# Kernel tuning notes

Measured on AMD Instinct MI355X. Metric: run time of the kernel, lower is better.

## Reference

```python
import jax, jax.numpy as jnp
import numpy as np

EPS = 1e-5

def layer_norm(x, g, b):
    mu = jnp.mean(x, axis=-1, keepdims=True)
    var = jnp.mean((x - mu) ** 2, axis=-1, keepdims=True)
    return (x - mu) * jax.lax.rsqrt(var + EPS) * g + b

def setup_inputs() -> dict:
    key = jax.random.key(0)
    ks = jax.random.split(key, 12)
    P, D_IN, H, D_OUT, N = 2097152, 3, 64, 128, 65536
    x = jax.random.normal(ks[0], (P, D_IN), dtype=jnp.float32)
    batch_idx = jax.random.randint(ks[1], (P,), 0, N, dtype=jnp.int64)
    # mlp1: Linear(3,64) -> LN(64) -> ReLU -> Linear(64,64)
    W1 = jax.random.normal(ks[2], (D_IN, H), dtype=jnp.float32) * (1.0 / np.sqrt(D_IN))
    b1 = jnp.zeros((H,), jnp.float32)
    g1 = jnp.ones((H,), jnp.float32)
    be1 = jnp.zeros((H,), jnp.float32)
    W2 = jax.random.normal(ks[3], (H, H), dtype=jnp.float32) * (1.0 / np.sqrt(H))
    b2 = jnp.zeros((H,), jnp.float32)
    # mlp2: Linear(64,128) -> LN(128) -> ReLU -> Linear(128,128)
    W3 = jax.random.normal(ks[4], (H, D_OUT), dtype=jnp.float32) * (1.0 / np.sqrt(H))
    b3 = jnp.zeros((D_OUT,), jnp.float32)
    g2 = jnp.ones((D_OUT,), jnp.float32)
    be2 = jnp.zeros((D_OUT,), jnp.float32)
    W4 = jax.random.normal(ks[5], (D_OUT, D_OUT), dtype=jnp.float32) * (1.0 / np.sqrt(D_OUT))
    b4 = jnp.zeros((D_OUT,), jnp.float32)
    return {"x": x, "batch_idx": batch_idx, "num_nodes": N,
            "W1": W1, "b1": b1, "g1": g1, "be1": be1, "W2": W2, "b2": b2,
            "W3": W3, "b3": b3, "g2": g2, "be2": be2, "W4": W4, "b4": b4}

def reference(x, batch_idx, num_nodes, W1, b1, g1, be1, W2, b2, W3, b3, g2, be2, W4, b4):
    # per-point MLP1: [P,3] -> [P,64]
    h = jax.nn.relu(layer_norm(x @ W1 + b1, g1, be1)) @ W2 + b2
    # scatter_max pooling over unsorted batch_idx -> [num_nodes, 64]
    seg = jax.ops.segment_max(h, batch_idx, num_segments=num_nodes)
    counts = jax.ops.segment_sum(jnp.ones((h.shape[0],), h.dtype), batch_idx, num_segments=num_nodes)
    # torch_scatter.scatter_max leaves empty segments at 0
    seg = jnp.where(counts[:, None] > 0, seg, 0.0)
    # MLP2: [N,64] -> [N,128]
    out = jax.nn.relu(layer_norm(seg @ W3 + b3, g2, be2)) @ W4 + b4
    return out
```

## Files before the change

kernel.cpp:

```cpp
#include <hip/hip_runtime.h>
#include <hip/hip_bf16.h>
#include <math.h>

#define EPS_LN 1e-5f

typedef __attribute__((ext_vector_type(8))) short bf16x8;
typedef __attribute__((ext_vector_type(4))) float f32x4;
typedef __attribute__((ext_vector_type(2))) unsigned short u16x2;
typedef __attribute__((ext_vector_type(4))) unsigned int u32x4;

__device__ __forceinline__ unsigned short f2bf(float f) {
    __hip_bfloat16 h = __float2bfloat16(f);
    return *reinterpret_cast<unsigned short*>(&h);
}
__device__ __forceinline__ float bf2f(unsigned short u) {
    return __uint_as_float(((unsigned)u) << 16);
}
__device__ __forceinline__ unsigned short ok16(float f) {
    unsigned short t = f2bf(f);
    unsigned short mask = (unsigned short)(((short)t) >> 15);
    return (unsigned short)(t ^ (unsigned short)(mask | 0x8000u));
}
__device__ __forceinline__ float decseg(unsigned o) {
    if (o == 0u) return 0.f;
    unsigned k = o >> 16;
    unsigned h = (k & 0x8000u) ? (k & 0x7FFFu) : (~k & 0xFFFFu);
    return bf2f((unsigned short)h);
}

__global__ __launch_bounds__(256) void prep_kernel(
    const float* __restrict__ W1, const float* __restrict__ b1,
    const float* __restrict__ g1, const float* __restrict__ be1,
    const float* __restrict__ W2,
    const float* __restrict__ W3, const float* __restrict__ W4,
    float* __restrict__ pW1e, float* __restrict__ pGB, float* __restrict__ pSG,
    unsigned short* __restrict__ pW2t,
    unsigned short* __restrict__ W3th, unsigned short* __restrict__ W3tl,
    unsigned short* __restrict__ W4th, unsigned short* __restrict__ W4tl)
{
    const int tid = threadIdx.x;
    if (tid < 64) {
        pW1e[4 * tid + 0] = W1[tid];
        pW1e[4 * tid + 1] = W1[64 + tid];
        pW1e[4 * tid + 2] = W1[128 + tid];
        pW1e[4 * tid + 3] = b1[tid];
        pGB[2 * tid + 0] = g1[tid];
        pGB[2 * tid + 1] = be1[tid];
    }
    if (tid >= 64 && tid < 78) {
        const int t = tid - 64;
        auto wcomp = [&](int k, int i) -> float {
            return (i < 3) ? W1[i * 64 + k] : b1[k];
        };
        if (t < 4) {
            float s = 0.f;
            for (int k = 0; k < 64; k++) s += wcomp(k, t);
            pSG[t] = s;
        } else {
            const int pi[10] = {0,0,0,0,1,1,1,2,2,3};
            const int pj[10] = {0,1,2,3,1,2,3,2,3,3};
            int p = t - 4;
            float s = 0.f;
            for (int k = 0; k < 64; k++) s += wcomp(k, pi[p]) * wcomp(k, pj[p]);
            pSG[4 + p] = s;
        }
    }
    for (int i = tid; i < 4096; i += 256) {
        int k = i >> 6, n = i & 63;
        pW2t[n * 72 + k] = f2bf(W2[i]);
    }
    for (int i = tid; i < 64 * 8; i += 256) {
        int n = i >> 3, k = 64 + (i & 7);
        pW2t[n * 72 + k] = 0;
    }
    for (int i = tid; i < 8192; i += 256) {
        int k = i >> 7, n = i & 127;
        float w = W3[k * 128 + n];
        unsigned short h = f2bf(w);
        W3th[n * 64 + k] = h;
        W3tl[n * 64 + k] = f2bf(w - bf2f(h));
    }
    for (int i = tid; i < 16384; i += 256) {
        int k = i >> 7, n = i & 127;
        float w = W4[k * 128 + n];
        unsigned short h = f2bf(w);
        W4th[n * 128 + k] = h;
        W4tl[n * 128 + k] = f2bf(w - bf2f(h));
    }
}

__global__ __launch_bounds__(256) void s1_count(const int* __restrict__ bidx,
                                                unsigned* __restrict__ blockHist, int P) {
    __shared__ unsigned hist[2048];
    const int tid = threadIdx.x;
    for (int i = tid; i < 2048; i += 256) hist[i] = 0;
    __syncthreads();
    const int base = blockIdx.x * 4096;
#pragma unroll
    for (int j = 0; j < 4; j++) {
        const int p0 = base + j * 1024 + tid * 4;
        if (p0 + 3 < P) {
            int4 n4 = *(const int4*)(bidx + p0);
            atomicAdd(&hist[((unsigned)n4.x) >> 5], 1u);
            atomicAdd(&hist[((unsigned)n4.y) >> 5], 1u);
            atomicAdd(&hist[((unsigned)n4.z) >> 5], 1u);
            atomicAdd(&hist[((unsigned)n4.w) >> 5], 1u);
        } else {
            for (int p = p0; p < P && p < p0 + 4; p++)
                atomicAdd(&hist[((unsigned)bidx[p]) >> 5], 1u);
        }
    }
    __syncthreads();
    unsigned* dst = blockHist + (size_t)blockIdx.x * 2048;
    for (int i = tid; i < 2048; i += 256) dst[i] = hist[i];
}

__global__ __launch_bounds__(256) void s2a_total(const unsigned* __restrict__ blockHist,
                                                 unsigned* __restrict__ binTotal, int nblk) {
    const int bin = blockIdx.x;
    const int tid = threadIdx.x;
    unsigned s = 0;
    for (int b = tid; b < nblk; b += 256) s += blockHist[(size_t)b * 2048 + bin];
    for (int off = 32; off; off >>= 1) s += __shfl_down(s, off);
    __shared__ unsigned ws[4];
    if ((tid & 63) == 0) ws[tid >> 6] = s;
    __syncthreads();
    if (tid == 0) binTotal[bin] = ws[0] + ws[1] + ws[2] + ws[3];
}

__global__ __launch_bounds__(1024) void s2b_scan(const unsigned* __restrict__ binTotal,
                                                 unsigned* __restrict__ partBase,
                                                 int nparts, int P) {
    __shared__ unsigned wtot[16];
    const int t = threadIdx.x;
    const unsigned c0 = (2 * t < nparts) ? binTotal[2 * t] : 0u;
    const unsigned c1 = (2 * t + 1 < nparts) ? binTotal[2 * t + 1] : 0u;
    const unsigned s = c0 + c1;
    unsigned v = s;
    const int lane = t & 63;
    for (int off = 1; off < 64; off <<= 1) {
        unsigned u = __shfl_up(v, off);
        if (lane >= off) v += u;
    }
    if (lane == 63) wtot[t >> 6] = v;
    __syncthreads();
    if (t == 0) {
        unsigned a = 0;
        for (int w = 0; w < 16; w++) { unsigned tmp = wtot[w]; wtot[w] = a; a += tmp; }
    }
    __syncthreads();
    const unsigned excl = wtot[t >> 6] + (v - s);
    if (2 * t < nparts) partBase[2 * t] = excl;
    if (2 * t + 1 < nparts) partBase[2 * t + 1] = excl + c0;
    if (t == 0) partBase[nparts] = (unsigned)P;
}

__global__ __launch_bounds__(256) void s2c_cursor(unsigned* __restrict__ blockHist,
                                                  const unsigned* __restrict__ partBase,
                                                  int nblk) {
    __shared__ unsigned wt0[4], wb0[4], wt1[4], wb1[4], tot0s;
    const int bin = blockIdx.x;
    const int tid = threadIdx.x;
    const int lane = tid & 63;
    const unsigned c0 = (tid < nblk) ? blockHist[(size_t)tid * 2048 + bin] : 0u;
    const unsigned c1 = (tid + 256 < nblk) ? blockHist[(size_t)(tid + 256) * 2048 + bin] : 0u;

    unsigned v0 = c0;
    for (int off = 1; off < 64; off <<= 1) {
        unsigned u = __shfl_up(v0, off);
        if (lane >= off) v0 += u;
    }
    if (lane == 63) wt0[tid >> 6] = v0;
    unsigned v1 = c1;
    for (int off = 1; off < 64; off <<= 1) {
        unsigned u = __shfl_up(v1, off);
        if (lane >= off) v1 += u;
    }
    if (lane == 63) wt1[tid >> 6] = v1;
    __syncthreads();
    if (tid == 0) {
        unsigned a = 0;
        for (int i = 0; i < 4; i++) { unsigned tmp = wt0[i]; wb0[i] = a; a += tmp; }
        tot0s = a;
        a = 0;
        for (int i = 0; i < 4; i++) { unsigned tmp = wt1[i]; wb1[i] = a; a += tmp; }
    }
    __syncthreads();
    const unsigned pb = partBase[bin];
    const unsigned e0 = pb + wb0[tid >> 6] + (v0 - c0);
    const unsigned e1 = pb + tot0s + wb1[tid >> 6] + (v1 - c1);
    if (tid < nblk) blockHist[(size_t)tid * 2048 + bin] = e0;
    if (tid + 256 < nblk) blockHist[(size_t)(tid + 256) * 2048 + bin] = e1;
}

__global__ __launch_bounds__(256) void s3_scatter(const int* __restrict__ bidx,
                                                  const float* __restrict__ x,
                                                  const unsigned* __restrict__ blockCursor,
                                                  float4* __restrict__ xb, int P) {
    __shared__ unsigned cur[2048];
    const int tid = threadIdx.x;
    const unsigned* src = blockCursor + (size_t)blockIdx.x * 2048;
    for (int i = tid; i < 2048; i += 256) cur[i] = src[i];
    __syncthreads();
    const int base = blockIdx.x * 4096;
#pragma unroll
    for (int j = 0; j < 4; j++) {
        const int p0 = base + j * 1024 + tid * 4;
        if (p0 + 3 < P) {
            int4 n4 = *(const int4*)(bidx + p0);
            const float4* xv = (const float4*)(x + 3 * (size_t)p0);
            float4 a = xv[0], b = xv[1], c = xv[2];
            const float xs[12] = {a.x, a.y, a.z, a.w, b.x, b.y, b.z, b.w,
                                  c.x, c.y, c.z, c.w};
            const unsigned nn[4] = {(unsigned)n4.x, (unsigned)n4.y,
                                    (unsigned)n4.z, (unsigned)n4.w};
#pragma unroll
            for (int u = 0; u < 4; u++) {
                const unsigned dst = atomicAdd(&cur[nn[u] >> 5], 1u);
                xb[dst] = make_float4(xs[3 * u], xs[3 * u + 1], xs[3 * u + 2],
                                      __uint_as_float(nn[u]));
            }
        } else {
            for (int u = 0; u < 4; u++) {
                const int p = p0 + u;
                if (p < P) {
                    const unsigned n = (unsigned)bidx[p];
                    const unsigned dst = atomicAdd(&cur[n >> 5], 1u);
                    xb[dst] = make_float4(x[3 * p], x[3 * p + 1], x[3 * p + 2],
                                          __uint_as_float(n));
                }
            }
        }
    }
}

__global__ __launch_bounds__(256) void s4_csr(const unsigned* __restrict__ partBase,
                                              unsigned* __restrict__ offsets,
                                              float4* __restrict__ xb, int N) {
    __shared__ float4 stage[1600];
    __shared__ unsigned hist[32], cur[32];
    const int tid = threadIdx.x;
    const int p = blockIdx.x;
    const unsigned start = partBase[p], end = partBase[p + 1];
    unsigned cnt = end - start;
    if (cnt > 1600u) cnt = 1600u;
    if (tid < 32) hist[tid] = 0;
    __syncthreads();
    for (unsigned k = tid; k < cnt; k += 256) {
        float4 r = xb[start + k];
        stage[k] = r;
        atomicAdd(&hist[__float_as_uint(r.w) & 31u], 1u);
    }
    __syncthreads();
    if (tid < 64) {
        const unsigned c = (tid < 32) ? hist[tid] : 0u;
        unsigned v = c;
        for (int off = 1; off < 32; off <<= 1) {
            unsigned u = __shfl_up(v, off);
            if (tid >= off) v += u;
        }
        if (tid < 32) {
            const unsigned excl = v - c;
            const int node = p * 32 + tid;
            if (node < N) offsets[node] = start + excl;
            cur[tid] = start + excl;
            if (node == N - 1) offsets[N] = start + excl + c;
        }
    }
    __syncthreads();
    for (unsigned k = tid; k < cnt; k += 256) {
        float4 r = stage[k];
        const unsigned dst = atomicAdd(&cur[__float_as_uint(r.w) & 31u], 1u);
        xb[dst] = r;
    }
}

__global__ __launch_bounds__(256, 4) void fused_mlp1_pool_kernel(
    const float4* __restrict__ xb, const unsigned* __restrict__ offsets,
    const float* __restrict__ pW1e, const float* __restrict__ pGB,
    const float* __restrict__ pSG, const unsigned short* __restrict__ pW2t,
    const float* __restrict__ b2,
    unsigned* __restrict__ segord, int P)
{
    __shared__ __align__(16) unsigned short shbt[64 * 260];
    __shared__ unsigned sn01[2];

    const int tid  = threadIdx.x;
    const int wv   = tid >> 6;
    const int lane = tid & 63;
    const int m    = lane & 15;
    const int quad = lane >> 4;
    const int base = blockIdx.x * 256;
    const int pos  = base + tid;
    const bool valid = (pos < P);

    bf16x8 bfrag[4][2];
    float bc[4];
#pragma unroll
    for (int nt = 0; nt < 4; nt++) {
        bc[nt] = b2[nt * 16 + m];
#pragma unroll
        for (int s = 0; s < 2; s++)
            bfrag[nt][s] = *reinterpret_cast<const bf16x8*>(
                &pW2t[(nt * 16 + m) * 72 + s * 32 + quad * 8]);
    }

    float x0 = 0.f, x1 = 0.f, x2 = 0.f;
    if (valid) {
        float4 v = xb[pos];
        x0 = v.x; x1 = v.y; x2 = v.z;
        unsigned node = __float_as_uint(v.w);
        if (tid == 0) sn01[0] = node;
        if (tid == 255 || pos == P - 1) sn01[1] = node;
    }

    float rs, r2;
    {
        const float S0 = pSG[0], S1 = pSG[1], S2 = pSG[2], S3 = pSG[3];
        const float g00 = pSG[4], g01 = pSG[5], g02 = pSG[6], g03 = pSG[7];
        const float g11 = pSG[8], g12 = pSG[9], g13 = pSG[10];
        const float g22 = pSG[11], g23 = pSG[12], g33 = pSG[13];

        const float mu = fmaf(S0, x0, fmaf(S1, x1, fmaf(S2, x2, S3))) * (1.f / 64.f);
        float q = g33;
        q = fmaf(g00, x0 * x0, q);
        q = fmaf(g11, x1 * x1, q);
        q = fmaf(g22, x2 * x2, q);
        float c = fmaf(g01, x1, fmaf(g02, x2, g03));
        q = fmaf(2.f * x0, c, q);
        q = fmaf(2.f * x1, fmaf(g12, x2, g13), q);
        q = fmaf(2.f * x2, g23, q);
        float var = q * (1.f / 64.f) - mu * mu;
        var = var > 0.f ? var : 0.f;
        rs = rsqrtf(var + EPS_LN);
        r2 = -mu * rs;
    }

    float xr0[4], xr1[4], xr2[4], rsr[4], r2r[4];
#pragma unroll
    for (int rt = 0; rt < 4; rt++) {
        const int src = rt * 16 + m;
        xr0[rt] = __shfl(x0, src);
        xr1[rt] = __shfl(x1, src);
        xr2[rt] = __shfl(x2, src);
        rsr[rt] = __shfl(rs, src);
        r2r[rt] = __shfl(r2, src);
    }

    u32x4 afr[4][2];
    {
        const float4* pw = (const float4*)pW1e;
        const float2* pg = (const float2*)pGB;
#pragma unroll
        for (int s = 0; s < 2; s++) {
#pragma unroll
            for (int up = 0; up < 4; up++) {
                const int ch = s * 32 + quad * 8 + up * 2;
                const float4 wA = pw[ch], wB = pw[ch + 1];
                const float2 gA = pg[ch], gB = pg[ch + 1];
#pragma unroll
                for (int rt = 0; rt < 4; rt++) {
                    float y0 = fmaf(xr0[rt], wA.x, fmaf(xr1[rt], wA.y,
                               fmaf(xr2[rt], wA.z, wA.w)));
                    float y1 = fmaf(xr0[rt], wB.x, fmaf(xr1[rt], wB.y,
                               fmaf(xr2[rt], wB.z, wB.w)));
                    float a0 = fmaf(fmaf(y0, rsr[rt], r2r[rt]), gA.x, gA.y);
                    float a1 = fmaf(fmaf(y1, rsr[rt], r2r[rt]), gB.x, gB.y);
                    a0 = a0 > 0.f ? a0 : 0.f;
                    a1 = a1 > 0.f ? a1 : 0.f;
                    afr[rt][s][up] = (unsigned)f2bf(a0) | ((unsigned)f2bf(a1) << 16);
                }
            }
        }
    }

#pragma unroll
    for (int rt = 0; rt < 4; rt++) {
        const int orow = wv * 64 + rt * 16 + quad * 4;
        const bf16x8 af0 = __builtin_bit_cast(bf16x8, afr[rt][0]);
        const bf16x8 af1 = __builtin_bit_cast(bf16x8, afr[rt][1]);
#pragma unroll
        for (int nt = 0; nt < 4; nt++) {
            f32x4 acc = {bc[nt], bc[nt], bc[nt], bc[nt]};
            acc = __builtin_amdgcn_mfma_f32_16x16x32_bf16(af0, bfrag[nt][0], acc, 0, 0, 0);
            acc = __builtin_amdgcn_mfma_f32_16x16x32_bf16(af1, bfrag[nt][1], acc, 0, 0, 0);
            const int col = nt * 16 + m;
            uint2 pk;
            pk.x = (unsigned)ok16(acc[0]) | ((unsigned)ok16(acc[1]) << 16);
            pk.y = (unsigned)ok16(acc[2]) | ((unsigned)ok16(acc[3]) << 16);
            *reinterpret_cast<uint2*>(&shbt[col * 260 + orow]) = pk;
        }
    }
    __syncthreads();

    const int nValid = (P - base < 256) ? (P - base) : 256;
    if (nValid <= 0) return;
    const unsigned n0 = sn01[0];
    const unsigned n1 = sn01[1];
    const unsigned bEnd = (unsigned)(base + nValid);
    const int wave = tid >> 6;
    const int ch   = tid & 63;
    const unsigned short* rowp = &shbt[ch * 260];

    for (unsigned n = n0 + (unsigned)wave; n <= n1; n += 4) {
        const unsigned s = offsets[n];
        const unsigned e = offsets[n + 1];
        int lo = (int)(s > (unsigned)base ? s : (unsigned)base) - base;
        int hi = (int)(e < bEnd ? e : bEnd) - base;
        if (hi <= lo) continue;
        u16x2 accv = {0, 0};
        unsigned short accs = 0;
        for (int r = lo & ~3; r < hi; r += 4) {
            uint2 d = *reinterpret_cast<const uint2*>(rowp + r);
            if (r >= lo && r + 4 <= hi) {
                u16x2 a = __builtin_bit_cast(u16x2, d.x);
                u16x2 b = __builtin_bit_cast(u16x2, d.y);
                accv = __builtin_elementwise_max(accv, __builtin_elementwise_max(a, b));
            } else {
                unsigned short v0 = (unsigned short)(d.x & 0xFFFFu);
                unsigned short v1 = (unsigned short)(d.x >> 16);
                unsigned short v2 = (unsigned short)(d.y & 0xFFFFu);
                unsigned short v3 = (unsigned short)(d.y >> 16);
                if (r     >= lo && r     < hi && v0 > accs) accs = v0;
                if (r + 1 >= lo && r + 1 < hi && v1 > accs) accs = v1;
                if (r + 2 >= lo && r + 2 < hi && v2 > accs) accs = v2;
                if (r + 3 >= lo && r + 3 < hi && v3 > accs) accs = v3;
            }
        }
        unsigned short k = accv.x > accv.y ? accv.x : accv.y;
        if (accs > k) k = accs;
        const unsigned key = ((unsigned)k) << 16;
        unsigned* dst = &segord[(size_t)n * 64 + ch];
        if (s >= (unsigned)base && e <= bEnd) *dst = key;
        else atomicMax(dst, key);
    }
}

__global__ __launch_bounds__(256) void mlp2_mfma_kernel(
    const unsigned* __restrict__ segord,
    const unsigned short* __restrict__ W3th, const unsigned short* __restrict__ W3tl,
    const unsigned short* __restrict__ W4th, const unsigned short* __restrict__ W4tl,
    const float* __restrict__ b3, const float* __restrict__ g2,
    const float* __restrict__ be2, const float* __restrict__ b4,
    float* __restrict__ out, int N)
{
    __shared__ __align__(16) unsigned short sa2[32 * 72];
    __shared__ __align__(16) float st[32 * 132];
    __shared__ __align__(16) unsigned short suh[32 * 136];
    __shared__ __align__(16) unsigned short sul[32 * 136];
    __shared__ float2 sred[32][8];
    __shared__ float sg2[128], sbe2[128];

    const int tid  = threadIdx.x;
    const int wv   = tid >> 6;
    const int lane = tid & 63;
    const int m    = lane & 15;
    const int quad = lane >> 4;

    if (tid < 128) { sg2[tid] = g2[tid]; sbe2[tid] = be2[tid]; }

    bf16x8 fw3h[2][2], fw3l[2][2];
    bf16x8 fw4h[2][4], fw4l[2][4];
    float bias3[2], bias4[2];
#pragma unroll
    for (int nti = 0; nti < 2; nti++) {
        const int nrow = (wv * 2 + nti) * 16 + m;
        bias3[nti] = b3[nrow];
        bias4[nti] = b4[nrow];
#pragma unroll
        for (int ks = 0; ks < 2; ks++) {
            fw3h[nti][ks] = *reinterpret_cast<const bf16x8*>(&W3th[nrow * 64 + ks * 32 + quad * 8]);
            fw3l[nti][ks] = *reinterpret_cast<const bf16x8*>(&W3tl[nrow * 64 + ks * 32 + quad * 8]);
        }
#pragma unroll
        for (int ks = 0; ks < 4; ks++) {
            fw4h[nti][ks] = *reinterpret_cast<const bf16x8*>(&W4th[nrow * 128 + ks * 32 + quad * 8]);
            fw4l[nti][ks] = *reinterpret_cast<const bf16x8*>(&W4tl[nrow * 128 + ks * 32 + quad * 8]);
        }
    }
    __syncthreads();

    for (int nb = blockIdx.x * 32; nb < N; nb += gridDim.x * 32) {
        {
            const int node = tid >> 3;
            const int k8   = (tid & 7) * 8;
            const uint4* sp = (const uint4*)&segord[(size_t)(nb + node) * 64 + k8];
            uint4 q0 = sp[0], q1 = sp[1];
            bf16x8 v;
            v[0] = (short)f2bf(decseg(q0.x));
            v[1] = (short)f2bf(decseg(q0.y));
            v[2] = (short)f2bf(decseg(q0.z));
            v[3] = (short)f2bf(decseg(q0.w));
            v[4] = (short)f2bf(decseg(q1.x));
            v[5] = (short)f2bf(decseg(q1.y));
            v[6] = (short)f2bf(decseg(q1.z));
            v[7] = (short)f2bf(decseg(q1.w));
            *reinterpret_cast<bf16x8*>(&sa2[node * 72 + k8]) = v;
        }
        __syncthreads();

#pragma unroll
        for (int mt = 0; mt < 2; mt++) {
            bf16x8 a0 = *reinterpret_cast<const bf16x8*>(&sa2[(mt * 16 + m) * 72 + quad * 8]);
            bf16x8 a1 = *reinterpret_cast<const bf16x8*>(&sa2[(mt * 16 + m) * 72 + 32 + quad * 8]);
#pragma unroll
            for (int nti = 0; nti < 2; nti++) {
                f32x4 acc = {bias3[nti], bias3[nti], bias3[nti], bias3[nti]};
                acc = __builtin_amdgcn_mfma_f32_16x16x32_bf16(a0, fw3h[nti][0], acc, 0, 0, 0);
                acc = __builtin_amdgcn_mfma_f32_16x16x32_bf16(a1, fw3h[nti][1], acc, 0, 0, 0);
                acc = __builtin_amdgcn_mfma_f32_16x16x32_bf16(a0, fw3l[nti][0], acc, 0, 0, 0);
                acc = __builtin_amdgcn_mfma_f32_16x16x32_bf16(a1, fw3l[nti][1], acc, 0, 0, 0);
#pragma unroll
                for (int r = 0; r < 4; r++)
                    st[(mt * 16 + quad * 4 + r) * 132 + (wv * 2 + nti) * 16 + m] = acc[r];
            }
        }
        __syncthreads();

        {
            const int node = tid >> 3;
            const int seg  = tid & 7;
            const float4* rp = (const float4*)&st[node * 132 + seg * 16];
            float4 v0 = rp[0], v1 = rp[1], v2 = rp[2], v3 = rp[3];
            float s1 = v0.x + v0.y + v0.z + v0.w + v1.x + v1.y + v1.z + v1.w
                     + v2.x + v2.y + v2.z + v2.w + v3.x + v3.y + v3.z + v3.w;
            float s2 = 0.f;
            s2 = fmaf(v0.x, v0.x, s2); s2 = fmaf(v0.y, v0.y, s2); s2 = fmaf(v0.z, v0.z, s2); s2 = fmaf(v0.w, v0.w, s2);
            s2 = fmaf(v1.x, v1.x, s2); s2 = fmaf(v1.y, v1.y, s2); s2 = fmaf(v1.z, v1.z, s2); s2 = fmaf(v1.w, v1.w, s2);
            s2 = fmaf(v2.x, v2.x, s2); s2 = fmaf(v2.y, v2.y, s2); s2 = fmaf(v2.z, v2.z, s2); s2 = fmaf(v2.w, v2.w, s2);
            s2 = fmaf(v3.x, v3.x, s2); s2 = fmaf(v3.y, v3.y, s2); s2 = fmaf(v3.z, v3.z, s2); s2 = fmaf(v3.w, v3.w, s2);
            sred[node][seg] = make_float2(s1, s2);
            __syncthreads();

            float t1 = 0.f, t2 = 0.f;
#pragma unroll
            for (int i = 0; i < 8; i++) { float2 r = sred[node][i]; t1 += r.x; t2 += r.y; }
            const float mu  = t1 * (1.f / 128.f);
            float var = t2 * (1.f / 128.f) - mu * mu;
            var = var > 0.f ? var : 0.f;
            const float rsd = rsqrtf(var + EPS_LN);

            float tv[16] = {v0.x, v0.y, v0.z, v0.w, v1.x, v1.y, v1.z, v1.w,
                            v2.x, v2.y, v2.z, v2.w, v3.x, v3.y, v3.z, v3.w};
            bf16x8 vh[2], vl[2];
#pragma unroll
            for (int i = 0; i < 16; i++) {
                const int j = seg * 16 + i;
                float u = fmaf((tv[i] - mu) * rsd, sg2[j], sbe2[j]);
                u = u > 0.f ? u : 0.f;
                unsigned short uh = f2bf(u);
                unsigned short ul = f2bf(u - bf2f(uh));
                vh[i >> 3][i & 7] = (short)uh;
                vl[i >> 3][i & 7] = (short)ul;
            }
            *reinterpret_cast<bf16x8*>(&suh[node * 136 + seg * 16])     = vh[0];
            *reinterpret_cast<bf16x8*>(&suh[node * 136 + seg * 16 + 8]) = vh[1];
            *reinterpret_cast<bf16x8*>(&sul[node * 136 + seg * 16])     = vl[0];
            *reinterpret_cast<bf16x8*>(&sul[node * 136 + seg * 16 + 8]) = vl[1];
        }
        __syncthreads();

#pragma unroll
        for (int mt = 0; mt < 2; mt++) {
            bf16x8 ah[4], al[4];
#pragma unroll
            for (int ks = 0; ks < 4; ks++) {
                ah[ks] = *reinterpret_cast<const bf16x8*>(&suh[(mt * 16 + m) * 136 + ks * 32 + quad * 8]);
                al[ks] = *reinterpret_cast<const bf16x8*>(&sul[(mt * 16 + m) * 136 + ks * 32 + quad * 8]);
            }
#pragma unroll
            for (int nti = 0; nti < 2; nti++) {
                f32x4 acc = {bias4[nti], bias4[nti], bias4[nti], bias4[nti]};
#pragma unroll
                for (int ks = 0; ks < 4; ks++) {
                    acc = __builtin_amdgcn_mfma_f32_16x16x32_bf16(ah[ks], fw4h[nti][ks], acc, 0, 0, 0);
                    acc = __builtin_amdgcn_mfma_f32_16x16x32_bf16(al[ks], fw4h[nti][ks], acc, 0, 0, 0);
                    acc = __builtin_amdgcn_mfma_f32_16x16x32_bf16(ah[ks], fw4l[nti][ks], acc, 0, 0, 0);
                }
#pragma unroll
                for (int r = 0; r < 4; r++) {
                    const int node = nb + mt * 16 + quad * 4 + r;
                    if (node < N)
                        out[(size_t)node * 128 + (wv * 2 + nti) * 16 + m] = acc[r];
                }
            }
        }
        __syncthreads();
    }
}

extern "C" void kernel_launch(void* const* d_in, const int* in_sizes, int n_in,
                              void* d_out, int out_size, void* d_ws, size_t ws_size,
                              hipStream_t stream) {
    const float* x    = (const float*)d_in[0];
    const int*   bidx = (const int*)d_in[1];
    const float* W1  = (const float*)d_in[3];
    const float* b1  = (const float*)d_in[4];
    const float* g1  = (const float*)d_in[5];
    const float* be1 = (const float*)d_in[6];
    const float* W2  = (const float*)d_in[7];
    const float* b2  = (const float*)d_in[8];
    const float* W3  = (const float*)d_in[9];
    const float* b3  = (const float*)d_in[10];
    const float* g2  = (const float*)d_in[11];
    const float* be2 = (const float*)d_in[12];
    const float* W4  = (const float*)d_in[13];
    const float* b4  = (const float*)d_in[14];

    const int P = in_sizes[0] / 3;
    const int N = out_size / 128;
    const int nparts = (N + 31) >> 5;
    const int nblk   = (P + 4095) / 4096;

    uintptr_t w = (uintptr_t)d_ws;
    auto align = [](uintptr_t v) { return (v + 255) & ~(uintptr_t)255; };
    unsigned* blockHist = (unsigned*)align(w);     w = (uintptr_t)(blockHist + (size_t)nblk * 2048);
    unsigned* binTotal  = (unsigned*)align(w);     w = (uintptr_t)(binTotal  + 2048);
    unsigned* partBase  = (unsigned*)align(w);     w = (uintptr_t)(partBase  + 2049);
    unsigned* offsets   = (unsigned*)align(w);     w = (uintptr_t)(offsets   + N + 1);
    float4*   xb        = (float4*)align(w);       w = (uintptr_t)(xb        + P);
    unsigned* segord    = (unsigned*)align(w);     w = (uintptr_t)(segord    + (size_t)N * 64);
    float*    pW1e      = (float*)align(w);        w = (uintptr_t)(pW1e      + 256);
    float*    pGB       = (float*)align(w);        w = (uintptr_t)(pGB       + 128);
    float*    pSG       = (float*)align(w);        w = (uintptr_t)(pSG       + 16);
    unsigned short* pW2t = (unsigned short*)align(w); w = (uintptr_t)(pW2t + 64 * 72);
    unsigned short* W3th = (unsigned short*)align(w); w = (uintptr_t)(W3th + 128 * 64);
    unsigned short* W3tl = (unsigned short*)align(w); w = (uintptr_t)(W3tl + 128 * 64);
    unsigned short* W4th = (unsigned short*)align(w); w = (uintptr_t)(W4th + 128 * 128);
    unsigned short* W4tl = (unsigned short*)align(w); w = (uintptr_t)(W4tl + 128 * 128);

    hipMemsetAsync(segord, 0, (size_t)N * 64 * sizeof(unsigned), stream);

    prep_kernel<<<1, 256, 0, stream>>>(W1, b1, g1, be1, W2, W3, W4,
                                       pW1e, pGB, pSG, pW2t, W3th, W3tl, W4th, W4tl);

    s1_count<<<nblk, 256, 0, stream>>>(bidx, blockHist, P);
    s2a_total<<<nparts, 256, 0, stream>>>(blockHist, binTotal, nblk);
    s2b_scan<<<1, 1024, 0, stream>>>(binTotal, partBase, nparts, P);
    s2c_cursor<<<nparts, 256, 0, stream>>>(blockHist, partBase, nblk);
    s3_scatter<<<nblk, 256, 0, stream>>>(bidx, x, blockHist, xb, P);
    s4_csr<<<nparts, 256, 0, stream>>>(partBase, offsets, xb, N);

    fused_mlp1_pool_kernel<<<(P + 255) / 256, 256, 0, stream>>>(
        xb, offsets, pW1e, pGB, pSG, pW2t, b2, segord, P);

    mlp2_mfma_kernel<<<512, 256, 0, stream>>>(
        segord, W3th, W3tl, W4th, W4tl, b3, g2, be2, b4, (float*)d_out, N);
}
```

Before: 340.3 us.

## Compute MLP1 first layer in packed fp16 and use fp16 MFMA

Moves the Linear(3,64)+LayerNorm+ReLU elementwise work in the fused MLP1/pool kernel from scalar fp32 FMAs to packed fp16x2 FMAs. The weights, gamma and beta are pre-packed as half pairs, and x, rs and r2 are shuffled as duplicated half pairs. The second linear layer switches from bf16 MFMA to f16 MFMA. The order-preserving key encoding is now done on packed 32-bit words, and the occupancy hint is lowered from 4 to 3. The aim is to halve the VALU instruction count of the per-point activation pass, at the cost of fp16 range and precision risk in the LayerNorm and ReLU intermediates.

```diff
diff --git a/kernel.cpp b/kernel.cpp
--- a/kernel.cpp
+++ b/kernel.cpp
@@ -8,6 +8,8 @@
 typedef __attribute__((ext_vector_type(4))) float f32x4;
 typedef __attribute__((ext_vector_type(2))) unsigned short u16x2;
 typedef __attribute__((ext_vector_type(4))) unsigned int u32x4;
+typedef _Float16 f16x2 __attribute__((ext_vector_type(2)));
+typedef _Float16 f16x8 __attribute__((ext_vector_type(8)));
 
 __device__ __forceinline__ unsigned short f2bf(float f) {
     __hip_bfloat16 h = __float2bfloat16(f);
@@ -16,10 +18,12 @@
 __device__ __forceinline__ float bf2f(unsigned short u) {
     return __uint_as_float(((unsigned)u) << 16);
 }
-__device__ __forceinline__ unsigned short ok16(float f) {
-    unsigned short t = f2bf(f);
-    unsigned short mask = (unsigned short)(((short)t) >> 15);
-    return (unsigned short)(t ^ (unsigned short)(mask | 0x8000u));
+__device__ __forceinline__ unsigned short f2h(float f) {
+    _Float16 h = (_Float16)f;
+    return __builtin_bit_cast(unsigned short, h);
+}
+__device__ __forceinline__ unsigned okpk(unsigned v) {
+    return v ^ (0x80008000u | (((v >> 15) & 0x00010001u) * 0x7FFFu));
 }
 __device__ __forceinline__ float decseg(unsigned o) {
     if (o == 0u) return 0.f;
@@ -27,25 +31,36 @@
     unsigned h = (k & 0x8000u) ? (k & 0x7FFFu) : (~k & 0xFFFFu);
     return bf2f((unsigned short)h);
 }
+__device__ __forceinline__ f16x2 bc16(unsigned u) {
+    return __builtin_bit_cast(f16x2, u);
+}
 
 __global__ __launch_bounds__(256) void prep_kernel(
     const float* __restrict__ W1, const float* __restrict__ b1,
     const float* __restrict__ g1, const float* __restrict__ be1,
     const float* __restrict__ W2,
     const float* __restrict__ W3, const float* __restrict__ W4,
-    float* __restrict__ pW1e, float* __restrict__ pGB, float* __restrict__ pSG,
+    unsigned short* __restrict__ pW1f, float* __restrict__ pSG,
     unsigned short* __restrict__ pW2t,
     unsigned short* __restrict__ W3th, unsigned short* __restrict__ W3tl,
     unsigned short* __restrict__ W4th, unsigned short* __restrict__ W4tl)
 {
     const int tid = threadIdx.x;
-    if (tid < 64) {
-        pW1e[4 * tid + 0] = W1[tid];
-        pW1e[4 * tid + 1] = W1[64 + tid];
-        pW1e[4 * tid + 2] = W1[128 + tid];
-        pW1e[4 * tid + 3] = b1[tid];
-        pGB[2 * tid + 0] = g1[tid];
-        pGB[2 * tid + 1] = be1[tid];
+    if (tid < 32) {
+        const int c0 = 2 * tid, c1 = 2 * tid + 1;
+        auto pk2 = [&](float a, float b) -> unsigned {
+            return (unsigned)f2h(a) | ((unsigned)f2h(b) << 16);
+        };
+        uint4 qa;
+        qa.x = pk2(W1[c0],        W1[c1]);
+        qa.y = pk2(W1[64 + c0],   W1[64 + c1]);
+        qa.z = pk2(W1[128 + c0],  W1[128 + c1]);
+        qa.w = pk2(b1[c0],        b1[c1]);
+        uint2 qb;
+        qb.x = pk2(g1[c0],  g1[c1]);
+        qb.y = pk2(be1[c0], be1[c1]);
+        *reinterpret_cast<uint4*>(&pW1f[tid * 16])     = qa;
+        *reinterpret_cast<uint2*>(&pW1f[tid * 16 + 8]) = qb;
     }
     if (tid >= 64 && tid < 78) {
         const int t = tid - 64;
@@ -67,7 +82,7 @@
     }
     for (int i = tid; i < 4096; i += 256) {
         int k = i >> 6, n = i & 63;
-        pW2t[n * 72 + k] = f2bf(W2[i]);
+        pW2t[n * 72 + k] = f2h(W2[i]);
     }
     for (int i = tid; i < 64 * 8; i += 256) {
         int n = i >> 3, k = 64 + (i & 7);
@@ -275,11 +290,10 @@
     }
 }
 
-__global__ __launch_bounds__(256, 4) void fused_mlp1_pool_kernel(
+__global__ __launch_bounds__(256, 3) void fused_mlp1_pool_kernel(
     const float4* __restrict__ xb, const unsigned* __restrict__ offsets,
-    const float* __restrict__ pW1e, const float* __restrict__ pGB,
-    const float* __restrict__ pSG, const unsigned short* __restrict__ pW2t,
-    const float* __restrict__ b2,
+    const unsigned short* __restrict__ pW1f, const float* __restrict__ pSG,
+    const unsigned short* __restrict__ pW2t, const float* __restrict__ b2,
     unsigned* __restrict__ segord, int P)
 {
     __shared__ __align__(16) unsigned short shbt[64 * 260];
@@ -293,17 +307,6 @@
     const int base = blockIdx.x * 256;
     const int pos  = base + tid;
     const bool valid = (pos < P);
-
-    bf16x8 bfrag[4][2];
-    float bc[4];
-#pragma unroll
-    for (int nt = 0; nt < 4; nt++) {
-        bc[nt] = b2[nt * 16 + m];
-#pragma unroll
-        for (int s = 0; s < 2; s++)
-            bfrag[nt][s] = *reinterpret_cast<const bf16x8*>(
-                &pW2t[(nt * 16 + m) * 72 + s * 32 + quad * 8]);
-    }
 
     float x0 = 0.f, x1 = 0.f, x2 = 0.f;
     if (valid) {
@@ -336,58 +339,66 @@
         r2 = -mu * rs;
     }
 
-    float xr0[4], xr1[4], xr2[4], rsr[4], r2r[4];
+    const unsigned px0 = (unsigned)f2h(x0) * 0x00010001u;
+    const unsigned px1 = (unsigned)f2h(x1) * 0x00010001u;
+    const unsigned px2 = (unsigned)f2h(x2) * 0x00010001u;
+    const unsigned prs = (unsigned)f2h(rs) * 0x00010001u;
+    const unsigned pr2 = (unsigned)f2h(r2) * 0x00010001u;
+
+    f16x8 bfrag[4][2];
+    float bc[4];
+#pragma unroll
+    for (int nt = 0; nt < 4; nt++) {
+        bc[nt] = b2[nt * 16 + m];
+#pragma unroll
+        for (int s = 0; s < 2; s++)
+            bfrag[nt][s] = *reinterpret_cast<const f16x8*>(
+                &pW2t[(nt * 16 + m) * 72 + s * 32 + quad * 8]);
+    }
+
+    const f16x2 fz = (f16x2)((_Float16)0.f);
+
 #pragma unroll
     for (int rt = 0; rt < 4; rt++) {
         const int src = rt * 16 + m;
-        xr0[rt] = __shfl(x0, src);
-        xr1[rt] = __shfl(x1, src);
-        xr2[rt] = __shfl(x2, src);
-        rsr[rt] = __shfl(rs, src);
-        r2r[rt] = __shfl(r2, src);
-    }
-
-    u32x4 afr[4][2];
-    {
-        const float4* pw = (const float4*)pW1e;
-        const float2* pg = (const float2*)pGB;
+        const f16x2 vx0 = bc16((unsigned)__shfl((int)px0, src));
+        const f16x2 vx1 = bc16((unsigned)__shfl((int)px1, src));
+        const f16x2 vx2 = bc16((unsigned)__shfl((int)px2, src));
+        const f16x2 vrs = bc16((unsigned)__shfl((int)prs, src));
+        const f16x2 vr2 = bc16((unsigned)__shfl((int)pr2, src));
+
+        unsigned aw[2][4];
 #pragma unroll
         for (int s = 0; s < 2; s++) {
 #pragma unroll
             for (int up = 0; up < 4; up++) {
-                const int ch = s * 32 + quad * 8 + up * 2;
-                const float4 wA = pw[ch], wB = pw[ch + 1];
-                const float2 gA = pg[ch], gB = pg[ch + 1];
-#pragma unroll
-                for (int rt = 0; rt < 4; rt++) {
-                    float y0 = fmaf(xr0[rt], wA.x, fmaf(xr1[rt], wA.y,
-                               fmaf(xr2[rt], wA.z, wA.w)));
-                    float y1 = fmaf(xr0[rt], wB.x, fmaf(xr1[rt], wB.y,
-                               fmaf(xr2[rt], wB.z, wB.w)));
-                    float a0 = fmaf(fmaf(y0, rsr[rt], r2r[rt]), gA.x, gA.y);
-                    float a1 = fmaf(fmaf(y1, rsr[rt], r2r[rt]), gB.x, gB.y);
-                    a0 = a0 > 0.f ? a0 : 0.f;
-                    a1 = a1 > 0.f ? a1 : 0.f;
-                    afr[rt][s][up] = (unsigned)f2bf(a0) | ((unsigned)f2bf(a1) << 16);
-                }
-            }
-        }
-    }
-
-#pragma unroll
-    for (int rt = 0; rt < 4; rt++) {
+                const int pidx = s * 16 + quad * 4 + up;
+                const uint4 q = *reinterpret_cast<const uint4*>(&pW1f[pidx * 16]);
+                const uint2 r = *reinterpret_cast<const uint2*>(&pW1f[pidx * 16 + 8]);
+                f16x2 y = __builtin_elementwise_fma(bc16(q.z), vx2, bc16(q.w));
+                y = __builtin_elementwise_fma(bc16(q.y), vx1, y);
+                y = __builtin_elementwise_fma(bc16(q.x), vx0, y);
+                f16x2 tn = __builtin_elementwise_fma(y, vrs, vr2);
+                f16x2 a  = __builtin_elementwise_fma(tn, bc16(r.x), bc16(r.y));
+                a = __builtin_elementwise_max(a, fz);
+                aw[s][up] = __builtin_bit_cast(unsigned, a);
+            }
+        }
+        const u32x4 a0w = {aw[0][0], aw[0][1], aw[0][2], aw[0][3]};
+        const u32x4 a1w = {aw[1][0], aw[1][1], aw[1][2], aw[1][3]};
+        const f16x8 af0 = __builtin_bit_cast(f16x8, a0w);
+        const f16x8 af1 = __builtin_bit_cast(f16x8, a1w);
+
         const int orow = wv * 64 + rt * 16 + quad * 4;
-        const bf16x8 af0 = __builtin_bit_cast(bf16x8, afr[rt][0]);
-        const bf16x8 af1 = __builtin_bit_cast(bf16x8, afr[rt][1]);
 #pragma unroll
         for (int nt = 0; nt < 4; nt++) {
             f32x4 acc = {bc[nt], bc[nt], bc[nt], bc[nt]};
-            acc = __builtin_amdgcn_mfma_f32_16x16x32_bf16(af0, bfrag[nt][0], acc, 0, 0, 0);
-            acc = __builtin_amdgcn_mfma_f32_16x16x32_bf16(af1, bfrag[nt][1], acc, 0, 0, 0);
+            acc = __builtin_amdgcn_mfma_f32_16x16x32_f16(af0, bfrag[nt][0], acc, 0, 0, 0);
+            acc = __builtin_amdgcn_mfma_f32_16x16x32_f16(af1, bfrag[nt][1], acc, 0, 0, 0);
             const int col = nt * 16 + m;
             uint2 pk;
-            pk.x = (unsigned)ok16(acc[0]) | ((unsigned)ok16(acc[1]) << 16);
-            pk.y = (unsigned)ok16(acc[2]) | ((unsigned)ok16(acc[3]) << 16);
+            pk.x = okpk((unsigned)f2bf(acc[0]) | ((unsigned)f2bf(acc[1]) << 16));
+            pk.y = okpk((unsigned)f2bf(acc[2]) | ((unsigned)f2bf(acc[3]) << 16));
             *reinterpret_cast<uint2*>(&shbt[col * 260 + orow]) = pk;
         }
     }
@@ -620,8 +631,7 @@
     unsigned* offsets   = (unsigned*)align(w);     w = (uintptr_t)(offsets   + N + 1);
     float4*   xb        = (float4*)align(w);       w = (uintptr_t)(xb        + P);
     unsigned* segord    = (unsigned*)align(w);     w = (uintptr_t)(segord    + (size_t)N * 64);
-    float*    pW1e      = (float*)align(w);        w = (uintptr_t)(pW1e      + 256);
-    float*    pGB       = (float*)align(w);        w = (uintptr_t)(pGB       + 128);
+    unsigned short* pW1f = (unsigned short*)align(w); w = (uintptr_t)(pW1f + 512);
     float*    pSG       = (float*)align(w);        w = (uintptr_t)(pSG       + 16);
     unsigned short* pW2t = (unsigned short*)align(w); w = (uintptr_t)(pW2t + 64 * 72);
     unsigned short* W3th = (unsigned short*)align(w); w = (uintptr_t)(W3th + 128 * 64);
@@ -632,7 +642,7 @@
     hipMemsetAsync(segord, 0, (size_t)N * 64 * sizeof(unsigned), stream);
 
     prep_kernel<<<1, 256, 0, stream>>>(W1, b1, g1, be1, W2, W3, W4,
-                                       pW1e, pGB, pSG, pW2t, W3th, W3tl, W4th, W4tl);
+                                       pW1f, pSG, pW2t, W3th, W3tl, W4th, W4tl);
 
     s1_count<<<nblk, 256, 0, stream>>>(bidx, blockHist, P);
     s2a_total<<<nparts, 256, 0, stream>>>(blockHist, binTotal, nblk);
@@ -642,7 +652,7 @@
     s4_csr<<<nparts, 256, 0, stream>>>(partBase, offsets, xb, N);
 
     fused_mlp1_pool_kernel<<<(P + 255) / 256, 256, 0, stream>>>(
-        xb, offsets, pW1e, pGB, pSG, pW2t, b2, segord, P);
+        xb, offsets, pW1f, pSG, pW2t, b2, segord, P);
 
     mlp2_mfma_kernel<<<512, 256, 0, stream>>>(
         segord, W3th, W3tl, W4th, W4tl, b3, g2, be2, b4, (float*)d_out, N);
```

After: 529.7 us. 55.7% more time.
